# Kernel tuning notes

Hardware: AMD Instinct MI355X
Metric: run time of the kernel (lower is better)

Reference implementation:

```python
import jax, jax.numpy as jnp
import numpy as np

L, B, H = 4096, 32, 512


def setup_inputs() -> dict:
    key = jax.random.key(0)
    k1, k2, k3, k4 = jax.random.split(key, 4)
    query = jax.random.normal(k1, (B, H), dtype=jnp.float32)
    key_val = jax.random.normal(k2, (L, B, H), dtype=jnp.float32)
    # torch Linear(2H, H, bias=False): weight is (H, 2H); we store transposed (2H, H)
    W = jax.random.normal(k3, (2 * H, H), dtype=jnp.float32) * (1.0 / np.sqrt(2 * H))
    v = jax.random.normal(k4, (H,), dtype=jnp.float32)
    return {"query": query, "key_val": key_val, "W": W, "v": v}


def reference(query, key_val, W, v):
    # concat([expand(query), key], -1) @ W == query @ W_q + key @ W_k
    Wq, Wk = W[:H], W[H:]                       # each (H, H)
    q_proj = query @ Wq                          # (B, H)
    k_proj = jnp.einsum('lbi,ih->lbh', key_val, Wk)  # (L, B, H)
    energy = jnp.tanh(q_proj[None, :, :] + k_proj)   # (L, B, H)
    scores = jnp.einsum('h,lbh->bl', v, energy)      # (B, L)
    return jax.nn.softmax(scores, axis=1)[:, None, :]  # (B, 1, L)
```

## Files before the change

kernel.cpp:

```cpp
#include <hip/hip_runtime.h>
#include <hip/hip_bf16.h>
#include <stdint.h>

#define L_DIM 4096
#define B_DIM 32
#define H_DIM 512
#define M_DIM (L_DIM * B_DIM)
#define K_DIM H_DIM

typedef _Float16 half8 __attribute__((ext_vector_type(8)));
typedef __fp16 fp16x2 __attribute__((ext_vector_type(2)));
typedef float floatx4 __attribute__((ext_vector_type(4)));

__device__ __forceinline__ float tanh_fast(float x) {
  float e = __builtin_amdgcn_exp2f(x * 2.88539008177793f);
  return 1.0f - 2.0f * __builtin_amdgcn_rcpf(e + 1.0f);
}

__device__ __forceinline__ uint2 pack4(const float4& f) {
  const fp16x2 p0 = __builtin_amdgcn_cvt_pkrtz(f.x, f.y);
  const fp16x2 p1 = __builtin_amdgcn_cvt_pkrtz(f.z, f.w);
  uint2 u;
  u.x = __builtin_bit_cast(unsigned, p0);
  u.y = __builtin_bit_cast(unsigned, p1);
  return u;
}

__device__ __forceinline__ void gload_lds16(const float* g, float* l) {
  __builtin_amdgcn_global_load_lds(
      (__attribute__((address_space(1))) void*)g,
      (__attribute__((address_space(3))) void*)l, 16, 0, 0);
}

__global__ __launch_bounds__(512) void prep_kernel(const float* __restrict__ query,
                                                   const float* __restrict__ W,
                                                   float* __restrict__ qp,
                                                   _Float16* __restrict__ W2) {
  __shared__ float4 qred[512];
  if (blockIdx.x < 64) {
    const int t = blockIdx.x * 512 + threadIdx.x;
    const int l15 = t & 15;
    const int q = (t >> 4) & 3;
    const int nc = (t >> 6) & 31;
    const int kt = t >> 11;
    const int n = nc * 16 + l15;
    const int kbase = H_DIM + kt * 32 + q * 8;
    half8 h;
#pragma unroll
    for (int j = 0; j < 8; ++j)
      h[j] = (_Float16)W[(size_t)(kbase + j) * H_DIM + n];
    *(half8*)(W2 + (size_t)t * 8) = h;
  } else {
    const int b = blockIdx.x - 64;
    const int tid = threadIdx.x;
    const int hx = tid & 127;
    const int ky = tid >> 7;
    const int h = hx * 4;
    const float* qrow = query + b * H_DIM + ky * 128;
    const float* wrow = W + (size_t)(ky * 128) * H_DIM + h;
    float4 acc = make_float4(0.f, 0.f, 0.f, 0.f);
#pragma unroll 8
    for (int i = 0; i < 128; ++i) {
      const float qv = qrow[i];
      const float4 w4 = *(const float4*)(wrow + (size_t)i * H_DIM);
      acc.x += qv * w4.x; acc.y += qv * w4.y;
      acc.z += qv * w4.z; acc.w += qv * w4.w;
    }
    qred[tid] = acc;
    __syncthreads();
    if (ky == 0) {
      const float4 a1 = qred[tid + 128], a2 = qred[tid + 256], a3 = qred[tid + 384];
      acc.x += a1.x + a2.x + a3.x;
      acc.y += a1.y + a2.y + a3.y;
      acc.z += a1.z + a2.z + a3.z;
      acc.w += a1.w + a2.w + a3.w;
      *(float4*)(qp + (size_t)b * H_DIM + h) = acc;
    }
  }
}

__global__ __launch_bounds__(512, 2) void fused_gemm_kernel(
    const float* __restrict__ key, const _Float16* __restrict__ W2,
    const float* __restrict__ qp, const float* __restrict__ v,
    float* __restrict__ scores) {
  __shared__ __align__(16) float As[3][128 * 32];
  __shared__ float swave[8 * 128];

  const int tid = threadIdx.x;
  const int lane = tid & 63;
  const int wn = tid >> 6;
  const int l15 = lane & 15;
  const int quad = lane >> 4;
  const int m0 = blockIdx.x * 128;

  const int arow = wn * 16 + (lane >> 3);
  const int lc = (lane & 7) ^ (lane >> 3);
  const float* ag0 = key + (size_t)(m0 + arow) * K_DIM + lc * 4;
  const float* ag1 = ag0 + (size_t)8 * K_DIM;
  float* lb0 = &As[0][0] + (wn * 2 + 0) * 256;
  float* lb1 = &As[0][0] + (wn * 2 + 1) * 256;

  const half8* bptr = (const half8*)W2 + (size_t)(wn * 4) * 64 + lane;

  floatx4 acc[8][4];
#pragma unroll
  for (int fm = 0; fm < 8; ++fm)
#pragma unroll
    for (int fn = 0; fn < 4; ++fn) acc[fm][fn] = (floatx4)0.0f;

  half8 bn[2][4];

  gload_lds16(ag0, lb0);
  gload_lds16(ag1, lb1);
  gload_lds16(ag0 + 32, lb0 + 4096);
  gload_lds16(ag1 + 32, lb1 + 4096);
#pragma unroll
  for (int fn = 0; fn < 4; ++fn) bn[0][fn] = bptr[fn * 64];
  bptr += 32 * 64;

#pragma unroll
  for (int kt = 0; kt < 16; ++kt) {
    if (kt < 15) {
      asm volatile("s_waitcnt vmcnt(6)" ::: "memory");
    } else {
      asm volatile("s_waitcnt vmcnt(4)" ::: "memory");
    }
    __builtin_amdgcn_sched_barrier(0);
    __builtin_amdgcn_s_barrier();
    __builtin_amdgcn_sched_barrier(0);

    if (kt < 14) {
      float* nb = lb0 + ((kt + 2) % 3) * 4096;
      gload_lds16(ag0 + (kt + 2) * 32, nb);
      gload_lds16(ag1 + (kt + 2) * 32, nb + 256);
    }
    if (kt < 15) {
#pragma unroll
      for (int fn = 0; fn < 4; ++fn) bn[(kt + 1) & 1][fn] = bptr[fn * 64];
      bptr += 32 * 64;
    }

    const float* buf = &As[kt % 3][0];
    half8 av[8];
#pragma unroll
    for (int fm = 0; fm < 8; ++fm) {
      const int rbase = (fm * 16 + l15) * 32;
      const float4 f0 = *(const float4*)(buf + rbase + (((2 * quad + 0) ^ (l15 & 7)) * 4));
      const float4 f1 = *(const float4*)(buf + rbase + (((2 * quad + 1) ^ (l15 & 7)) * 4));
      const uint2 u0 = pack4(f0);
      const uint2 u1 = pack4(f1);
      const uint4 uu = make_uint4(u0.x, u0.y, u1.x, u1.y);
      av[fm] = __builtin_bit_cast(half8, uu);
    }
#pragma unroll
    for (int fm = 0; fm < 8; ++fm)
#pragma unroll
      for (int fn = 0; fn < 4; ++fn)
        acc[fm][fn] = __builtin_amdgcn_mfma_f32_16x16x32_f16(av[fm], bn[kt & 1][fn],
                                                             acc[fm][fn], 0, 0, 0);
  }

  float vv[4];
#pragma unroll
  for (int fn = 0; fn < 4; ++fn) vv[fn] = v[wn * 64 + fn * 16 + l15];

#pragma unroll
  for (int fm = 0; fm < 8; ++fm) {
#pragma unroll
    for (int r = 0; r < 4; ++r) {
      const int mrow = fm * 16 + quad * 4 + r;
      const float* qrow = qp + (size_t)(mrow & 31) * H_DIM;
      float rs = 0.f;
#pragma unroll
      for (int fn = 0; fn < 4; ++fn) {
        const int n = wn * 64 + fn * 16 + l15;
        const float x = qrow[n] + acc[fm][fn][r];
        rs += vv[fn] * tanh_fast(x);
      }
      rs += __shfl_xor(rs, 1);
      rs += __shfl_xor(rs, 2);
      rs += __shfl_xor(rs, 4);
      rs += __shfl_xor(rs, 8);
      if (l15 == 0) swave[wn * 128 + mrow] = rs;
    }
  }
  __syncthreads();
  if (tid < 128) {
    float s = 0.f;
#pragma unroll
    for (int j = 0; j < 8; ++j) s += swave[j * 128 + tid];
    const int m = m0 + tid;
    scores[(size_t)(m & 31) * L_DIM + (m >> 5)] = s;
  }
}

__global__ __launch_bounds__(256) void softmax_kernel(const float* __restrict__ scores,
                                                      float* __restrict__ out) {
  const int b = blockIdx.x;
  const int t = threadIdx.x;
  const int lane = t & 63;
  const int w = t >> 6;
  __shared__ float redm[4], reds[4];
  const float* srow = scores + (size_t)b * L_DIM;
  float s[16];
#pragma unroll
  for (int i = 0; i < 16; ++i) s[i] = srow[t + i * 256];
  float mx = s[0];
#pragma unroll
  for (int i = 1; i < 16; ++i) mx = fmaxf(mx, s[i]);
#pragma unroll
  for (int off = 1; off < 64; off <<= 1) mx = fmaxf(mx, __shfl_xor(mx, off));
  if (lane == 0) redm[w] = mx;
  __syncthreads();
  mx = fmaxf(fmaxf(redm[0], redm[1]), fmaxf(redm[2], redm[3]));
  float sum = 0.f;
#pragma unroll
  for (int i = 0; i < 16; ++i) {
    s[i] = __builtin_amdgcn_exp2f((s[i] - mx) * 1.44269504f);
    sum += s[i];
  }
#pragma unroll
  for (int off = 1; off < 64; off <<= 1) sum += __shfl_xor(sum, off);
  if (lane == 0) reds[w] = sum;
  __syncthreads();
  const float inv = 1.0f / (reds[0] + reds[1] + reds[2] + reds[3]);
#pragma unroll
  for (int i = 0; i < 16; ++i) out[(size_t)b * L_DIM + t + i * 256] = s[i] * inv;
}

extern "C" void kernel_launch(void* const* d_in, const int* in_sizes, int n_in,
                              void* d_out, int out_size, void* d_ws, size_t ws_size,
                              hipStream_t stream) {
  const float* query = (const float*)d_in[0];
  const float* key   = (const float*)d_in[1];
  const float* W     = (const float*)d_in[2];
  const float* v     = (const float*)d_in[3];
  float* out = (float*)d_out;

  char* ws = (char*)d_ws;
  float* qp       = (float*)ws;
  float* scores   = (float*)(ws + 65536);
  _Float16* W2    = (_Float16*)(ws + 65536 + 524288);

  prep_kernel<<<96, 512, 0, stream>>>(query, W, qp, W2);
  fused_gemm_kernel<<<M_DIM / 128, 512, 0, stream>>>(key, W2, qp, v, scores);
  softmax_kernel<<<B_DIM, 256, 0, stream>>>(scores, out);
}
```

Measured before the change: 440.2 us.

## Halve GEMM M-tile to 64 rows with 4-stage LDS pipeline and higher occupancy

Shrinks the fused GEMM block tile from 128 to 64 rows, which halves the accumulator registers and allows 4 blocks per CU instead of 2. It also deepens the LDS ring for the key tiles from 3 to 4 stages and re-derives the vmcnt wait counts. Higher occupancy and a deeper prefetch are meant to hide the global load latency of this memory-bound key stream. The cost is that each block now reloads the full W2 operand for only half as many rows, which doubles B-operand traffic and the loads per MFMA. The hand-tuned wait counts risk being wrong.

```diff
diff --git a/kernel.cpp b/kernel.cpp
--- a/kernel.cpp
+++ b/kernel.cpp
@@ -31,6 +31,8 @@
       (__attribute__((address_space(1))) void*)g,
       (__attribute__((address_space(3))) void*)l, 16, 0, 0);
 }
+
+#define VM_WAIT(n) asm volatile("s_waitcnt vmcnt(" #n ")" ::: "memory")
 
 __global__ __launch_bounds__(512) void prep_kernel(const float* __restrict__ query,
                                                    const float* __restrict__ W,
@@ -79,60 +81,55 @@
   }
 }
 
-__global__ __launch_bounds__(512, 2) void fused_gemm_kernel(
+__global__ __launch_bounds__(512, 4) void fused_gemm_kernel(
     const float* __restrict__ key, const _Float16* __restrict__ W2,
     const float* __restrict__ qp, const float* __restrict__ v,
     float* __restrict__ scores) {
-  __shared__ __align__(16) float As[3][128 * 32];
-  __shared__ float swave[8 * 128];
+  __shared__ __align__(16) float As[4][64 * 32];
+  __shared__ float swave[8 * 64];
 
   const int tid = threadIdx.x;
   const int lane = tid & 63;
   const int wn = tid >> 6;
   const int l15 = lane & 15;
   const int quad = lane >> 4;
-  const int m0 = blockIdx.x * 128;
-
-  const int arow = wn * 16 + (lane >> 3);
-  const int lc = (lane & 7) ^ (lane >> 3);
-  const float* ag0 = key + (size_t)(m0 + arow) * K_DIM + lc * 4;
-  const float* ag1 = ag0 + (size_t)8 * K_DIM;
-  float* lb0 = &As[0][0] + (wn * 2 + 0) * 256;
-  float* lb1 = &As[0][0] + (wn * 2 + 1) * 256;
+  const int m0 = blockIdx.x * 64;
+
+  const int srow = tid >> 3;
+  const int lc = (tid & 7) ^ (srow & 7);
+  const float* ag = key + (size_t)(m0 + srow) * K_DIM + lc * 4;
+  float* lbase = &As[0][0] + wn * 256;
 
   const half8* bptr = (const half8*)W2 + (size_t)(wn * 4) * 64 + lane;
 
-  floatx4 acc[8][4];
-#pragma unroll
-  for (int fm = 0; fm < 8; ++fm)
+  floatx4 acc[4][4];
+#pragma unroll
+  for (int fm = 0; fm < 4; ++fm)
 #pragma unroll
     for (int fn = 0; fn < 4; ++fn) acc[fm][fn] = (floatx4)0.0f;
 
   half8 bn[2][4];
 
-  gload_lds16(ag0, lb0);
-  gload_lds16(ag1, lb1);
-  gload_lds16(ag0 + 32, lb0 + 4096);
-  gload_lds16(ag1 + 32, lb1 + 4096);
+  gload_lds16(ag, lbase);
+  gload_lds16(ag + 32, lbase + 2048);
+  gload_lds16(ag + 64, lbase + 4096);
 #pragma unroll
   for (int fn = 0; fn < 4; ++fn) bn[0][fn] = bptr[fn * 64];
   bptr += 32 * 64;
 
 #pragma unroll
   for (int kt = 0; kt < 16; ++kt) {
-    if (kt < 15) {
-      asm volatile("s_waitcnt vmcnt(6)" ::: "memory");
-    } else {
-      asm volatile("s_waitcnt vmcnt(4)" ::: "memory");
-    }
+    if (kt == 0)       VM_WAIT(6);
+    else if (kt == 1)  VM_WAIT(10);
+    else if (kt == 14) VM_WAIT(13);
+    else if (kt == 15) VM_WAIT(12);
+    else               VM_WAIT(14);
     __builtin_amdgcn_sched_barrier(0);
     __builtin_amdgcn_s_barrier();
     __builtin_amdgcn_sched_barrier(0);
 
-    if (kt < 14) {
-      float* nb = lb0 + ((kt + 2) % 3) * 4096;
-      gload_lds16(ag0 + (kt + 2) * 32, nb);
-      gload_lds16(ag1 + (kt + 2) * 32, nb + 256);
+    if (kt < 13) {
+      gload_lds16(ag + (kt + 3) * 32, lbase + ((kt + 3) & 3) * 2048);
     }
     if (kt < 15) {
 #pragma unroll
@@ -140,10 +137,10 @@
       bptr += 32 * 64;
     }
 
-    const float* buf = &As[kt % 3][0];
-    half8 av[8];
-#pragma unroll
-    for (int fm = 0; fm < 8; ++fm) {
+    const float* buf = &As[kt & 3][0];
+    half8 av[4];
+#pragma unroll
+    for (int fm = 0; fm < 4; ++fm) {
       const int rbase = (fm * 16 + l15) * 32;
       const float4 f0 = *(const float4*)(buf + rbase + (((2 * quad + 0) ^ (l15 & 7)) * 4));
       const float4 f1 = *(const float4*)(buf + rbase + (((2 * quad + 1) ^ (l15 & 7)) * 4));
@@ -153,7 +150,7 @@
       av[fm] = __builtin_bit_cast(half8, uu);
     }
 #pragma unroll
-    for (int fm = 0; fm < 8; ++fm)
+    for (int fm = 0; fm < 4; ++fm)
 #pragma unroll
       for (int fn = 0; fn < 4; ++fn)
         acc[fm][fn] = __builtin_amdgcn_mfma_f32_16x16x32_f16(av[fm], bn[kt & 1][fn],
@@ -165,7 +162,7 @@
   for (int fn = 0; fn < 4; ++fn) vv[fn] = v[wn * 64 + fn * 16 + l15];
 
 #pragma unroll
-  for (int fm = 0; fm < 8; ++fm) {
+  for (int fm = 0; fm < 4; ++fm) {
 #pragma unroll
     for (int r = 0; r < 4; ++r) {
       const int mrow = fm * 16 + quad * 4 + r;
@@ -181,14 +178,14 @@
       rs += __shfl_xor(rs, 2);
       rs += __shfl_xor(rs, 4);
       rs += __shfl_xor(rs, 8);
-      if (l15 == 0) swave[wn * 128 + mrow] = rs;
+      if (l15 == 0) swave[wn * 64 + mrow] = rs;
     }
   }
   __syncthreads();
-  if (tid < 128) {
+  if (tid < 64) {
     float s = 0.f;
 #pragma unroll
-    for (int j = 0; j < 8; ++j) s += swave[j * 128 + tid];
+    for (int j = 0; j < 8; ++j) s += swave[j * 64 + tid];
     const int m = m0 + tid;
     scores[(size_t)(m & 31) * L_DIM + (m >> 5)] = s;
   }
@@ -243,6 +240,6 @@
   _Float16* W2    = (_Float16*)(ws + 65536 + 524288);
 
   prep_kernel<<<96, 512, 0, stream>>>(query, W, qp, W2);
-  fused_gemm_kernel<<<M_DIM / 128, 512, 0, stream>>>(key, W2, qp, v, scores);
+  fused_gemm_kernel<<<M_DIM / 64, 512, 0, stream>>>(key, W2, qp, v, scores);
   softmax_kernel<<<B_DIM, 256, 0, stream>>>(scores, out);
 }
```

Result: faster. 428.8 us (-2.6%).
